# Kernel tuning notes

Hardware: AMD Instinct MI355X
Metric: run time of the kernel (lower is better)

Reference implementation:

```python
import jax, jax.numpy as jnp
import numpy as np

IS, OS, H = 168, 24, 256           # input window, output horizon, state_hsize
TAU, MAXIMUM = 0.1, 1.0            # tau parameter (non-grad) and series maximum
DILS = [[1, 4], [16, 64]]          # ResidualDRNN groups of dilations


def _lstm(x, wih, whh, bih, bhh):
    """Single-layer LSTM over time-major x: (T, B, C). PyTorch gate order i,f,g,o."""
    def step(carry, xt):
        h, c = carry
        g = xt @ wih.T + h @ whh.T + (bih + bhh)
        i, f, gg, o = jnp.split(g, 4, axis=-1)
        c = jax.nn.sigmoid(f) * c + jax.nn.sigmoid(i) * jnp.tanh(gg)
        h = jax.nn.sigmoid(o) * jnp.tanh(c)
        return (h, c), h
    h0 = jnp.zeros((x.shape[1], H), x.dtype)
    _, hs = jax.lax.scan(step, (h0, h0), x)
    return hs


def _dilated_lstm(x, d, p):
    """Standard DRNN layer: pad T to multiple of d, interleave time into batch, run LSTM."""
    T, B, C = x.shape
    n = -(-T // d)
    xp = jnp.pad(x, ((0, n * d - T), (0, 0), (0, 0)))
    hd = _lstm(xp.reshape(n, d * B, C), *p)
    return hd.reshape(n * d, B, H)[:T]


def _forward(train, init_lev_sm, lstm_params, nl_w, nl_b, sc_w, sc_b):
    B, T = train.shape
    a = jax.nn.sigmoid(init_lev_sm[0])            # lev_sms (idxs are all 0 -> same scalar)
    floor = TAU * MAXIMUM                          # tau * maximum
    # --- exponential-smoothing level recurrence (sequential) ---
    lev0 = jnp.maximum(train[:, 0], floor)
    def step(lev, xt):
        new = jnp.maximum(a * xt + (1.0 - a) * lev, floor)
        return new, new
    _, rest = jax.lax.scan(step, lev0, train[:, 1:].T)
    levs = jnp.concatenate([lev0[None], rest], axis=0).T   # [B, T]
    # --- windowed normalization ---
    w_idx = jnp.arange(IS - 1, T)                           # W = T - IS + 1 window ends
    in_win = train[:, (w_idx - IS + 1)[:, None] + jnp.arange(IS)[None, :]]
    in_win = (in_win / levs[:, w_idx][:, :, None]).transpose(1, 0, 2)    # [W, B, IS]
    o_idx = jnp.arange(IS - 1, T - OS)                      # W_out = T - OS - IS + 1
    out_win = train[:, (o_idx + 1)[:, None] + jnp.arange(OS)[None, :]]
    out_win = (out_win / levs[:, o_idx][:, :, None]).transpose(1, 0, 2)  # [W_out, B, OS]
    # --- ResidualDRNN stack on window_input[:-OS] (time-major: windows are the sequence) ---
    x = in_win[:-OS]
    li = 0
    for g, dils in enumerate(DILS):
        residual = x
        h = x
        for d in dils:
            h = _dilated_lstm(h, d, lstm_params[li])
            li += 1
        x = h + residual if g > 0 else h                    # dropout p=0 -> identity
    x = jnp.tanh(x @ nl_w.T + nl_b)                         # add_nl_layer
    pred = x @ sc_w.T + sc_b                                # scoring
    return pred, out_win


def setup_inputs() -> dict:
    key = jax.random.key(0)
    ks = list(jax.random.split(key, 32))
    B, T = 32, 1024
    inp = {
        "train": jax.random.uniform(ks[0], (B, T), jnp.float32, 0.05, 1.0),
        "val": jax.random.uniform(ks[1], (B, T), jnp.float32, 0.05, 1.0),
        "test": jax.random.uniform(ks[2], (B, T), jnp.float32, 0.05, 1.0),
        "idxs": jnp.zeros((B,), jnp.int32),
        "init_lev_sm": jnp.array([0.5], jnp.float32),
    }
    sizes = [IS, H, H, H]  # input feature size of each of the 4 DRNN layers
    k = 3
    s = 1.0 / np.sqrt(H)
    for i, cin in enumerate(sizes):
        inp[f"wih{i}"] = jax.random.uniform(ks[k], (4 * H, cin), jnp.float32, -s, s); k += 1
        inp[f"whh{i}"] = jax.random.uniform(ks[k], (4 * H, H), jnp.float32, -s, s); k += 1
        inp[f"bih{i}"] = jax.random.uniform(ks[k], (4 * H,), jnp.float32, -s, s); k += 1
        inp[f"bhh{i}"] = jax.random.uniform(ks[k], (4 * H,), jnp.float32, -s, s); k += 1
    inp["nl_w"] = jax.random.uniform(ks[k], (H, H), jnp.float32, -s, s); k += 1
    inp["nl_b"] = jnp.zeros((H,), jnp.float32)
    inp["sc_w"] = jax.random.uniform(ks[k], (OS, H), jnp.float32, -s, s); k += 1
    inp["sc_b"] = jnp.zeros((OS,), jnp.float32)
    return inp


def reference(train, val, test, idxs, init_lev_sm,
              wih0, whh0, bih0, bhh0, wih1, whh1, bih1, bhh1,
              wih2, whh2, bih2, bhh2, wih3, whh3, bih3, bhh3,
              nl_w, nl_b, sc_w, sc_b):
    lstm_params = [(wih0, whh0, bih0, bhh0), (wih1, whh1, bih1, bhh1),
                   (wih2, whh2, bih2, bhh2), (wih3, whh3, bih3, bhh3)]
    # training path (validating=False, testing=False): only `train` is used
    return _forward(train, init_lev_sm, lstm_params, nl_w, nl_b, sc_w, sc_b)
```

## Files before the change

kernel.cpp:

```cpp
#include <hip/hip_runtime.h>
#include <hip/hip_fp16.h>
#include <math.h>

#define TT 833
#define GDIM 1024

typedef _Float16 f16x8 __attribute__((ext_vector_type(8)));
typedef float    f32x4 __attribute__((ext_vector_type(4)));

#if __has_builtin(__builtin_amdgcn_rcpf)
__device__ __forceinline__ float frcp(float x){ return __builtin_amdgcn_rcpf(x); }
#else
__device__ __forceinline__ float frcp(float x){ return 1.f/x; }
#endif

#if __has_builtin(__builtin_amdgcn_sdot4)
__device__ __forceinline__ int sdot4(unsigned a, unsigned b, int c){
  return __builtin_amdgcn_sdot4((int)a, (int)b, c, false);
}
#else
__device__ __forceinline__ int sdot4(unsigned a, unsigned b, int c){
  int ai = (int)a, bi = (int)b;
  c += ((ai<<24)>>24)*((bi<<24)>>24);
  c += ((ai<<16)>>24)*((bi<<16)>>24);
  c += ((ai<<8)>>24)*((bi<<8)>>24);
  c += (ai>>24)*(bi>>24);
  return c;
}
#endif

__device__ __forceinline__ void lds_barrier(){
  asm volatile("s_waitcnt lgkmcnt(0)" ::: "memory");
  __builtin_amdgcn_s_barrier();
  __builtin_amdgcn_sched_barrier(0);
}


__global__ void levels_k(const float* __restrict__ train, const float* __restrict__ ism,
                         float* __restrict__ levs){
  int b = threadIdx.x;
  if (b >= 32) return;
  float a = 1.f/(1.f+expf(-ism[0]));
  const float4* tr4 = reinterpret_cast<const float4*>(train + b*1024);
  float4* lv4 = reinterpret_cast<float4*>(levs + b*1024);
  float lev = 0.f;
  for (int i = 0; i < 256; ++i){
    float4 v = tr4[i];
    float4 o;
    if (i == 0) o.x = lev = fmaxf(v.x, 0.1f);
    else        o.x = lev = fmaxf(fmaf(a, v.x, (1.f-a)*lev), 0.1f);
    o.y = lev = fmaxf(fmaf(a, v.y, (1.f-a)*lev), 0.1f);
    o.z = lev = fmaxf(fmaf(a, v.z, (1.f-a)*lev), 0.1f);
    o.w = lev = fmaxf(fmaf(a, v.w, (1.f-a)*lev), 0.1f);
    lv4[i] = o;
  }
}

__global__ void win_x_k(const float* __restrict__ train, const float* __restrict__ levs,
                        __half* __restrict__ x0){
  int idx = blockIdx.x*256 + threadIdx.x;
  int i = idx % 192;
  int r = idx / 192;
  int b = r & 31;
  int t = r >> 5;
  x0[idx] = (i < 168) ? __float2half(train[b*1024 + t + i] / levs[b*1024 + t + 167])
                      : __float2half(0.f);
}

__global__ void win_out_k(const float* __restrict__ train, const float* __restrict__ levs,
                          float* __restrict__ ow){
  int idx = blockIdx.x*256 + threadIdx.x;
  int o = idx % 24;
  int r = idx / 24;
  int b = r & 31;
  int t = r >> 5;
  ow[idx] = train[b*1024 + 168 + t + o] / levs[b*1024 + t + 167];
}

__global__ void permw_k(const float* __restrict__ wih, const float* __restrict__ bih,
                        const float* __restrict__ bhh, __half* __restrict__ wP,
                        float* __restrict__ bP, int K, int Kpad){
  int t = blockIdx.x;
  int g = ((t & 3) << 8) + (t >> 2);
  for (int k = threadIdx.x; k < Kpad; k += 256)
    wP[(size_t)t*Kpad + k] = (k < K) ? __float2half(wih[(size_t)g*K + k]) : __float2half(0.f);
  if (threadIdx.x == 0) bP[t] = bih[g] + bhh[g];
}

__global__ void cvth_k(const float* __restrict__ s, __half* __restrict__ d, int n){
  int i = blockIdx.x*256 + threadIdx.x;
  if (i < n) d[i] = __float2half(s[i]);
}

__global__ void packq_k(const float* __restrict__ w, uint4* __restrict__ wq,
                        float* __restrict__ sc){
  int t = blockIdx.x*256 + threadIdx.x;
  if (t >= 1024) return;
  int g = ((t & 3) << 8) + (t >> 2);
  const float* row = w + (size_t)g*256;
  float amax = 0.f;
  for (int k = 0; k < 256; ++k) amax = fmaxf(amax, fabsf(row[k]));
  amax = fmaxf(amax, 1e-20f);
  float s = amax/127.f, inv = 127.f/amax;
  sc[t] = s;
  for (int k16 = 0; k16 < 16; ++k16){
    union { uint4 u; signed char b[16]; } r;
    #pragma unroll
    for (int j = 0; j < 16; ++j){
      float q = rintf(row[k16*16 + j]*inv);
      q = fminf(fmaxf(q, -127.f), 127.f);
      r.b[j] = (signed char)q;
    }
    wq[(size_t)k16*1024 + t] = r.u;
  }
}

__global__ __launch_bounds__(512) void proj_mfma(
    const _Float16* __restrict__ A, const _Float16* __restrict__ W,
    const float* __restrict__ b1,
    void* __restrict__ C, int Mout, int K, int N, int dil, int act, int outHalf)
{
  __shared__ _Float16 As[256*40];
  __shared__ _Float16 Bs[128*40];
  const int tid = threadIdx.x;
  const int lane = tid & 63;
  const int w = tid >> 6, wr = w >> 1, wc = w & 1;
  const int m0 = blockIdx.y << 8, n0 = blockIdx.x << 7;

  const int rowA = tid >> 1;
  const int halfsel = tid & 1;
  int srcrow;
  {
    int m = m0 + rowA;
    if (dil == 0) srcrow = (m < Mout) ? m : -1;
    else {
      int rows = dil << 5;
      int jj = m / rows;
      int q = m - jj*rows;
      int t = jj*dil + (q >> 5);
      srcrow = (t < TT) ? ((t << 5) + (q & 31)) : -1;
    }
  }
  const int rowB = (tid & 255) >> 1;
  const int nrow = n0 + rowB;

  f32x4 acc[4][4];
  #pragma unroll
  for (int i = 0; i < 4; ++i)
    #pragma unroll
    for (int j = 0; j < 4; ++j) acc[i][j] = (f32x4){0.f,0.f,0.f,0.f};

  const int nkt = K >> 5;
  for (int kt = 0; kt < nkt; ++kt){
    const int k0 = (kt << 5) + halfsel*16;
    {
      union { uint4 u[2]; _Float16 h[16]; } tmp;
      if (srcrow >= 0){
        const uint4* s = reinterpret_cast<const uint4*>(A + (size_t)srcrow*K + k0);
        tmp.u[0] = s[0]; tmp.u[1] = s[1];
      } else {
        tmp.u[0] = make_uint4(0,0,0,0); tmp.u[1] = make_uint4(0,0,0,0);
      }
      uint4* dst = reinterpret_cast<uint4*>(&As[rowA*40 + halfsel*16]);
      dst[0] = tmp.u[0]; dst[1] = tmp.u[1];
    }
    if (tid < 256){
      const uint4* s = reinterpret_cast<const uint4*>(W + (size_t)nrow*K + k0);
      uint4* dst = reinterpret_cast<uint4*>(&Bs[rowB*40 + halfsel*16]);
      dst[0] = s[0]; dst[1] = s[1];
    }
    __syncthreads();
    {
      const int kg = lane >> 4, r16 = lane & 15;
      f16x8 af[4], bf[4];
      #pragma unroll
      for (int mi = 0; mi < 4; ++mi)
        af[mi] = *reinterpret_cast<const f16x8*>(&As[(wr*64 + mi*16 + r16)*40 + kg*8]);
      #pragma unroll
      for (int nj = 0; nj < 4; ++nj)
        bf[nj] = *reinterpret_cast<const f16x8*>(&Bs[(wc*64 + nj*16 + r16)*40 + kg*8]);
      #pragma unroll
      for (int mi = 0; mi < 4; ++mi)
        #pragma unroll
        for (int nj = 0; nj < 4; ++nj)
          acc[mi][nj] = __builtin_amdgcn_mfma_f32_16x16x32_f16(af[mi], bf[nj], acc[mi][nj], 0, 0, 0);
    }
    __syncthreads();
  }
  #pragma unroll
  for (int mi = 0; mi < 4; ++mi){
    #pragma unroll
    for (int p = 0; p < 4; ++p){
      int mrow = m0 + wr*64 + mi*16 + (lane >> 4)*4 + p;
      if (mrow >= Mout) continue;
      #pragma unroll
      for (int nj = 0; nj < 4; ++nj){
        int ncol = n0 + wc*64 + nj*16 + (lane & 15);
        float v = acc[mi][nj][p] + b1[ncol];
        if (act) v = tanhf(v);
        if (outHalf) reinterpret_cast<__half*>(C)[(size_t)mrow*N + ncol] = __float2half(v);
        else reinterpret_cast<float*>(C)[(size_t)mrow*N + ncol] = v;
      }
    }
  }
}

template<int NR>
__global__ __launch_bounds__(512, 1) void srecr2_k(
    const uint4* __restrict__ wq, const float* __restrict__ scale,
    const __half* __restrict__ Gin,
    __half* __restrict__ outh, float* __restrict__ outf,
    int nsteps, int d, int rowsTotal)
{
  __shared__ __align__(16) unsigned int hq[2][NR][64];
  const int tid = threadIdx.x;
  const int s = tid & 1;
  const int j = tid >> 1;
  const int q0 = blockIdx.x*NR;
  const float sg0 = scale[2*tid]*(1.f/127.f);
  const float sg1 = scale[2*tid + 1]*(1.f/127.f);
  uint4 w0_[16], w1_[16];
  #pragma unroll
  for (int kk = 0; kk < 16; ++kk){
    w0_[kk] = wq[(size_t)kk*1024 + 2*tid];
    w1_[kk] = wq[(size_t)kk*1024 + 2*tid + 1];
  }
  float c[NR];
  #pragma unroll
  for (int rr = 0; rr < NR; ++rr) c[rr] = 0.f;
  for (int e = tid; e < 2*NR*64; e += 512) (&hq[0][0][0])[e] = 0u;
  __syncthreads();

  for (int step = 0; step < nsteps; ++step){
    const int cur = step & 1;
    const __half2* gbase = reinterpret_cast<const __half2*>(
        Gin + ((size_t)step*rowsTotal + q0)*GDIM);
    #pragma unroll
    for (int rr = 0; rr < NR; ++rr){
      __half2 g2 = gbase[rr*512 + tid];
      float gin0 = __half2float(__low2half(g2));
      float gin1 = __half2float(__high2half(g2));
      int a00 = 0, a01 = 0, a10 = 0, a11 = 0;
      #pragma unroll
      for (int k16 = 0; k16 < 8; ++k16){
        uint4 ha = *reinterpret_cast<const uint4*>(&hq[cur][rr][4*k16]);
        a00 = sdot4(w0_[k16].x, ha.x, a00); a00 = sdot4(w0_[k16].y, ha.y, a00);
        a00 = sdot4(w0_[k16].z, ha.z, a00); a00 = sdot4(w0_[k16].w, ha.w, a00);
        a10 = sdot4(w1_[k16].x, ha.x, a10); a10 = sdot4(w1_[k16].y, ha.y, a10);
        a10 = sdot4(w1_[k16].z, ha.z, a10); a10 = sdot4(w1_[k16].w, ha.w, a10);
        uint4 hb = *reinterpret_cast<const uint4*>(&hq[cur][rr][4*(k16 + 8)]);
        a01 = sdot4(w0_[k16+8].x, hb.x, a01); a01 = sdot4(w0_[k16+8].y, hb.y, a01);
        a01 = sdot4(w0_[k16+8].z, hb.z, a01); a01 = sdot4(w0_[k16+8].w, hb.w, a01);
        a11 = sdot4(w1_[k16+8].x, hb.x, a11); a11 = sdot4(w1_[k16+8].y, hb.y, a11);
        a11 = sdot4(w1_[k16+8].w, hb.w, a11); a11 = sdot4(w1_[k16+8].z, hb.z, a11);
      }
      float p0 = fmaf((float)(a00 + a01), sg0, gin0);
      float p1 = fmaf((float)(a10 + a11), sg1, gin1);
      float px0 = s ? p0 + p0 : p0;
      float t0 = frcp(1.f + __expf(-px0));
      float a0v = s ? fmaf(2.f, t0, -1.f) : t0;
      float a1v = frcp(1.f + __expf(-p1));
      float b0 = __shfl_xor(a0v, 1);
      float b1 = __shfl_xor(a1v, 1);
      float iv = s ? b0 : a0v;
      float fv = s ? b1 : a1v;
      float gv = s ? a0v : b0;
      float ov = s ? a1v : b1;
      float cn = fmaf(fv, c[rr], iv*gv);
      c[rr] = cn;
      if (s == 0){
        float e2 = __expf(-2.f*cn);
        float h = ov*(1.f - e2)*frcp(1.f + e2);
        int qh = (int)rintf(h*127.f);
        reinterpret_cast<signed char*>(&hq[cur^1][rr][0])[j] = (signed char)qh;
        int q = q0 + rr;
        int tg = step*d + (q >> 5);
        if (tg < TT){
          size_t oi = ((size_t)tg*32 + (q & 31))*256 + j;
          outh[oi] = __float2half(h);
          if (outf) outf[oi] = h;
        }
      }
    }
    lds_barrier();
  }
}

template<int NR>
__global__ __launch_bounds__(1024) void srecq_k(
    const uint4* __restrict__ wq, const float* __restrict__ scale,
    const __half* __restrict__ Gin,
    __half* __restrict__ outh, const float* __restrict__ res,
    int nsteps, int d, int rowsTotal)
{
  __shared__ __align__(16) unsigned int hq[2][NR][64];
  const int tid = threadIdx.x;
  const int lane = tid & 63;
  const int base = lane & ~3;
  const int kg = tid & 3;
  const int j = tid >> 2;
  const int q0 = blockIdx.x*NR;
  const float sg = scale[tid]*(1.f/127.f);
  float c[NR];
  #pragma unroll
  for (int rr = 0; rr < NR; ++rr) c[rr] = 0.f;
  for (int e = tid; e < 2*NR*64; e += 1024) (&hq[0][0][0])[e] = 0u;
  __syncthreads();

  for (int step = 0; step < nsteps; ++step){
    const int cur = step & 1;
    float gin[NR];
    const __half* gbase = Gin + ((size_t)step*rowsTotal + q0)*GDIM;
    #pragma unroll
    for (int rr = 0; rr < NR; ++rr) gin[rr] = __half2float(gbase[rr*GDIM + tid]);
    int acc[NR];
    #pragma unroll
    for (int rr = 0; rr < NR; ++rr) acc[rr] = 0;
    #pragma unroll 4
    for (int k16 = 0; k16 < 16; ++k16){
      uint4 w = wq[(size_t)k16*1024 + tid];
      #pragma unroll
      for (int rr = 0; rr < NR; ++rr){
        uint4 h4 = *reinterpret_cast<const uint4*>(&hq[cur][rr][4*k16]);
        acc[rr] = sdot4(w.x, h4.x, acc[rr]);
        acc[rr] = sdot4(w.y, h4.y, acc[rr]);
        acc[rr] = sdot4(w.z, h4.z, acc[rr]);
        acc[rr] = sdot4(w.w, h4.w, acc[rr]);
      }
    }
    #pragma unroll
    for (int rr = 0; rr < NR; ++rr){
      float p = fmaf((float)acc[rr], sg, gin[rr]);
      float px = (kg == 2) ? p + p : p;
      float sv = frcp(1.f + __expf(-px));
      float a = (kg == 2) ? fmaf(2.f, sv, -1.f) : sv;
      float iv = __shfl(a, base + 0);
      float fv = __shfl(a, base + 1);
      float gv = __shfl(a, base + 2);
      float ov = __shfl(a, base + 3);
      float cn = fmaf(fv, c[rr], iv*gv);
      c[rr] = cn;
      float e2 = __expf(-2.f*cn);
      float h = ov*(1.f - e2)*frcp(1.f + e2);
      if (kg == 0){
        int qh = (int)rintf(h*127.f);
        reinterpret_cast<signed char*>(&hq[cur^1][rr][0])[j] = (signed char)qh;
        int q = q0 + rr;
        int tg = step*d + (q >> 5);
        if (tg < TT){
          size_t oi = ((size_t)tg*32 + (q & 31))*256 + j;
          outh[oi] = __float2half(h + res[oi]);
        }
      }
    }
    lds_barrier();
  }
}

__global__ __launch_bounds__(256) void sc_head(const __half* __restrict__ xt, const float* __restrict__ w,
                        const float* __restrict__ bias, float* __restrict__ outp, int M){
  __shared__ float arow[8][256];
  int m0 = blockIdx.x << 3;
  int tid = threadIdx.x;
  #pragma unroll
  for (int i = 0; i < 8; ++i){
    int e = tid + (i << 8);
    int r = e >> 8, k = e & 255;
    arow[r][k] = (m0 + r < M) ? __half2float(xt[(size_t)(m0 + r)*256 + k]) : 0.f;
  }
  __syncthreads();
  int r = tid >> 5, n = tid & 31;
  if (n < 24 && (m0 + r) < M){
    float acc = bias[n];
    const float* wr = w + n*256;
    #pragma unroll 8
    for (int k = 0; k < 256; ++k) acc = fmaf(arow[r][k], wr[k], acc);
    outp[(size_t)(m0 + r)*24 + n] = acc;
  }
}

extern "C" void kernel_launch(void* const* d_in, const int* in_sizes, int n_in,
                              void* d_out, int out_size, void* d_ws, size_t ws_size,
                              hipStream_t stream){
  const float* train = (const float*)d_in[0];
  const float* ism   = (const float*)d_in[4];
  const float* wih[4] = {(const float*)d_in[5], (const float*)d_in[9], (const float*)d_in[13], (const float*)d_in[17]};
  const float* whh[4] = {(const float*)d_in[6], (const float*)d_in[10], (const float*)d_in[14], (const float*)d_in[18]};
  const float* bih[4] = {(const float*)d_in[7], (const float*)d_in[11], (const float*)d_in[15], (const float*)d_in[19]};
  const float* bhh[4] = {(const float*)d_in[8], (const float*)d_in[12], (const float*)d_in[16], (const float*)d_in[20]};
  const float* nl_w = (const float*)d_in[21];
  const float* nl_b = (const float*)d_in[22];
  const float* sc_w = (const float*)d_in[23];
  const float* sc_b = (const float*)d_in[24];
  float* out = (float*)d_out;

  float* ws = (float*)d_ws;
  size_t off = 0;
  float* levs = ws + off;   off += 32768;
  uint4* wqk[4];
  for (int l = 0; l < 4; ++l){ wqk[l] = (uint4*)(ws + off); off += 65536; }
  float* sck[4];
  for (int l = 0; l < 4; ++l){ sck[l] = ws + off; off += 1024; }
  __half* wPh[4];
  for (int l = 0; l < 4; ++l){ wPh[l] = (__half*)(ws + off); off += 131072; }
  float* bP[4];
  for (int l = 0; l < 4; ++l){ bP[l] = ws + off; off += 1024; }
  __half* nlwh = (__half*)(ws + off); off += 32768;
  __half* x0h = (__half*)(ws + off);  off += (size_t)26656*192/2;
  __half* G   = (__half*)(ws + off);  off += (size_t)28672*1024/2;
  __half* h0h = (__half*)(ws + off);  off += (size_t)26656*256/2;
  __half* h1h = (__half*)(ws + off);  off += (size_t)26656*256/2;
  float*  h1f = ws + off;             off += (size_t)26656*256;
  __half* h2h = (__half*)(ws + off);  off += (size_t)26656*256/2;
  __half* xfh = (__half*)(ws + off);  off += (size_t)26656*256/2;
  __half* xth = (__half*)(ws + off);  off += (size_t)26656*256/2;
  (void)ws_size; (void)in_sizes; (void)n_in; (void)out_size;

  levels_k<<<1, 64, 0, stream>>>(train, ism, levs);
  win_x_k<<<19992, 256, 0, stream>>>(train, levs, x0h);
  win_out_k<<<2499, 256, 0, stream>>>(train, levs, out + 639744);
  const int Kin[4]  = {168, 256, 256, 256};
  const int Kpad[4] = {192, 256, 256, 256};
  for (int l = 0; l < 4; ++l){
    packq_k<<<4, 256, 0, stream>>>(whh[l], wqk[l], sck[l]);
    permw_k<<<1024, 256, 0, stream>>>(wih[l], bih[l], bhh[l], wPh[l], bP[l], Kin[l], Kpad[l]);
  }
  cvth_k<<<256, 256, 0, stream>>>(nl_w, nlwh, 65536);

  proj_mfma<<<dim3(8,105), 512, 0, stream>>>((const _Float16*)x0h, (const _Float16*)wPh[0], bP[0], G, 26656, 192, 1024, 0, 0, 1);
  srecr2_k<1><<<32, 512, 0, stream>>>(wqk[0], sck[0], G, h0h, nullptr, 833, 1, 32);
  proj_mfma<<<dim3(8,105), 512, 0, stream>>>((const _Float16*)h0h, (const _Float16*)wPh[1], bP[1], G, 26752, 256, 1024, 4, 0, 1);
  srecr2_k<1><<<128, 512, 0, stream>>>(wqk[1], sck[1], G, h1h, h1f, 209, 4, 128);
  proj_mfma<<<dim3(8,106), 512, 0, stream>>>((const _Float16*)h1h, (const _Float16*)wPh[2], bP[2], G, 27136, 256, 1024, 16, 0, 1);
  srecr2_k<2><<<256, 512, 0, stream>>>(wqk[2], sck[2], G, h2h, nullptr, 53, 16, 512);
  proj_mfma<<<dim3(8,112), 512, 0, stream>>>((const _Float16*)h2h, (const _Float16*)wPh[3], bP[3], G, 28672, 256, 1024, 64, 0, 1);
  srecq_k<8><<<256, 1024, 0, stream>>>(wqk[3], sck[3], G, xfh, h1f, 14, 64, 2048);
  proj_mfma<<<dim3(2,105), 512, 0, stream>>>((const _Float16*)xfh, (const _Float16*)nlwh, nl_b, xth, 26656, 256, 256, 0, 1, 1);
  sc_head<<<3332, 256, 0, stream>>>(xth, sc_w, sc_b, out, 26656);
}
```

Before: 1.613 ms.

## Compute all four LSTM gates per thread in recurrent kernel, halving block size

The recurrent int8-dot kernel now gives each of 256 threads one hidden unit with all four gates (i,f,g,o) held in registers, instead of 512 threads each handling two gates and exchanging them by cross-lane shuffles. This removes the shuffles and the idle half of threads in the cell-update tail, and every thread now writes h. The cost is twice as many weight registers per thread (64 uint4) and a longer serial dot-product chain per thread, with fewer waves available to hide latency on the sequential critical path.

```diff
diff --git a/kernel.cpp b/kernel.cpp
--- a/kernel.cpp
+++ b/kernel.cpp
@@ -206,80 +206,75 @@
 }
 
 template<int NR>
-__global__ __launch_bounds__(512, 1) void srecr2_k(
+__global__ __launch_bounds__(256, 1) void srecc_k(
     const uint4* __restrict__ wq, const float* __restrict__ scale,
     const __half* __restrict__ Gin,
     __half* __restrict__ outh, float* __restrict__ outf,
     int nsteps, int d, int rowsTotal)
 {
   __shared__ __align__(16) unsigned int hq[2][NR][64];
-  const int tid = threadIdx.x;
-  const int s = tid & 1;
-  const int j = tid >> 1;
+  const int t = threadIdx.x;
   const int q0 = blockIdx.x*NR;
-  const float sg0 = scale[2*tid]*(1.f/127.f);
-  const float sg1 = scale[2*tid + 1]*(1.f/127.f);
-  uint4 w0_[16], w1_[16];
-  #pragma unroll
-  for (int kk = 0; kk < 16; ++kk){
-    w0_[kk] = wq[(size_t)kk*1024 + 2*tid];
-    w1_[kk] = wq[(size_t)kk*1024 + 2*tid + 1];
-  }
+  float sg[4];
+  #pragma unroll
+  for (int g = 0; g < 4; ++g) sg[g] = scale[4*t + g]*(1.f/127.f);
+  uint4 w_[4][16];
+  #pragma unroll
+  for (int k = 0; k < 16; ++k)
+    #pragma unroll
+    for (int g = 0; g < 4; ++g)
+      w_[g][k] = wq[(size_t)k*1024 + 4*t + g];
   float c[NR];
   #pragma unroll
   for (int rr = 0; rr < NR; ++rr) c[rr] = 0.f;
-  for (int e = tid; e < 2*NR*64; e += 512) (&hq[0][0][0])[e] = 0u;
+  for (int e = t; e < 2*NR*64; e += 256) (&hq[0][0][0])[e] = 0u;
   __syncthreads();
 
   for (int step = 0; step < nsteps; ++step){
     const int cur = step & 1;
-    const __half2* gbase = reinterpret_cast<const __half2*>(
-        Gin + ((size_t)step*rowsTotal + q0)*GDIM);
     #pragma unroll
     for (int rr = 0; rr < NR; ++rr){
-      __half2 g2 = gbase[rr*512 + tid];
-      float gin0 = __half2float(__low2half(g2));
-      float gin1 = __half2float(__high2half(g2));
-      int a00 = 0, a01 = 0, a10 = 0, a11 = 0;
-      #pragma unroll
-      for (int k16 = 0; k16 < 8; ++k16){
-        uint4 ha = *reinterpret_cast<const uint4*>(&hq[cur][rr][4*k16]);
-        a00 = sdot4(w0_[k16].x, ha.x, a00); a00 = sdot4(w0_[k16].y, ha.y, a00);
-        a00 = sdot4(w0_[k16].z, ha.z, a00); a00 = sdot4(w0_[k16].w, ha.w, a00);
-        a10 = sdot4(w1_[k16].x, ha.x, a10); a10 = sdot4(w1_[k16].y, ha.y, a10);
-        a10 = sdot4(w1_[k16].z, ha.z, a10); a10 = sdot4(w1_[k16].w, ha.w, a10);
-        uint4 hb = *reinterpret_cast<const uint4*>(&hq[cur][rr][4*(k16 + 8)]);
-        a01 = sdot4(w0_[k16+8].x, hb.x, a01); a01 = sdot4(w0_[k16+8].y, hb.y, a01);
-        a01 = sdot4(w0_[k16+8].z, hb.z, a01); a01 = sdot4(w0_[k16+8].w, hb.w, a01);
-        a11 = sdot4(w1_[k16+8].x, hb.x, a11); a11 = sdot4(w1_[k16+8].y, hb.y, a11);
-        a11 = sdot4(w1_[k16+8].w, hb.w, a11); a11 = sdot4(w1_[k16+8].z, hb.z, a11);
-      }
-      float p0 = fmaf((float)(a00 + a01), sg0, gin0);
-      float p1 = fmaf((float)(a10 + a11), sg1, gin1);
-      float px0 = s ? p0 + p0 : p0;
-      float t0 = frcp(1.f + __expf(-px0));
-      float a0v = s ? fmaf(2.f, t0, -1.f) : t0;
-      float a1v = frcp(1.f + __expf(-p1));
-      float b0 = __shfl_xor(a0v, 1);
-      float b1 = __shfl_xor(a1v, 1);
-      float iv = s ? b0 : a0v;
-      float fv = s ? b1 : a1v;
-      float gv = s ? a0v : b0;
-      float ov = s ? a1v : b1;
+      const __half* gb = Gin + ((size_t)step*rowsTotal + q0 + rr)*GDIM + 4*t;
+      uint2 gu = *reinterpret_cast<const uint2*>(gb);
+      union { unsigned u; __half2 h2; } glo, ghi;
+      glo.u = gu.x; ghi.u = gu.y;
+      float gi = __half2float(__low2half(glo.h2));
+      float gf = __half2float(__high2half(glo.h2));
+      float gg = __half2float(__low2half(ghi.h2));
+      float go = __half2float(__high2half(ghi.h2));
+      int a0 = 0, a1 = 0, a2 = 0, a3 = 0;
+      #pragma unroll
+      for (int k = 0; k < 16; ++k){
+        uint4 h4 = *reinterpret_cast<const uint4*>(&hq[cur][rr][4*k]);
+        a0 = sdot4(w_[0][k].x, h4.x, a0); a0 = sdot4(w_[0][k].y, h4.y, a0);
+        a0 = sdot4(w_[0][k].z, h4.z, a0); a0 = sdot4(w_[0][k].w, h4.w, a0);
+        a1 = sdot4(w_[1][k].x, h4.x, a1); a1 = sdot4(w_[1][k].y, h4.y, a1);
+        a1 = sdot4(w_[1][k].z, h4.z, a1); a1 = sdot4(w_[1][k].w, h4.w, a1);
+        a2 = sdot4(w_[2][k].x, h4.x, a2); a2 = sdot4(w_[2][k].y, h4.y, a2);
+        a2 = sdot4(w_[2][k].z, h4.z, a2); a2 = sdot4(w_[2][k].w, h4.w, a2);
+        a3 = sdot4(w_[3][k].x, h4.x, a3); a3 = sdot4(w_[3][k].y, h4.y, a3);
+        a3 = sdot4(w_[3][k].z, h4.z, a3); a3 = sdot4(w_[3][k].w, h4.w, a3);
+      }
+      float pi = fmaf((float)a0, sg[0], gi);
+      float pf = fmaf((float)a1, sg[1], gf);
+      float pg = fmaf((float)a2, sg[2], gg);
+      float po = fmaf((float)a3, sg[3], go);
+      float iv = frcp(1.f + __expf(-pi));
+      float fv = frcp(1.f + __expf(-pf));
+      float gv = fmaf(2.f, frcp(1.f + __expf(-2.f*pg)), -1.f);
+      float ov = frcp(1.f + __expf(-po));
       float cn = fmaf(fv, c[rr], iv*gv);
       c[rr] = cn;
-      if (s == 0){
-        float e2 = __expf(-2.f*cn);
-        float h = ov*(1.f - e2)*frcp(1.f + e2);
-        int qh = (int)rintf(h*127.f);
-        reinterpret_cast<signed char*>(&hq[cur^1][rr][0])[j] = (signed char)qh;
-        int q = q0 + rr;
-        int tg = step*d + (q >> 5);
-        if (tg < TT){
-          size_t oi = ((size_t)tg*32 + (q & 31))*256 + j;
-          outh[oi] = __float2half(h);
-          if (outf) outf[oi] = h;
-        }
+      float e2 = __expf(-2.f*cn);
+      float h = ov*(1.f - e2)*frcp(1.f + e2);
+      int qh = (int)rintf(h*127.f);
+      reinterpret_cast<signed char*>(&hq[cur^1][rr][0])[t] = (signed char)qh;
+      int q = q0 + rr;
+      int tg = step*d + (q >> 5);
+      if (tg < TT){
+        size_t oi = ((size_t)tg*32 + (q & 31))*256 + t;
+        outh[oi] = __float2half(h);
+        if (outf) outf[oi] = h;
       }
     }
     lds_barrier();
@@ -428,11 +423,11 @@
   cvth_k<<<256, 256, 0, stream>>>(nl_w, nlwh, 65536);
 
   proj_mfma<<<dim3(8,105), 512, 0, stream>>>((const _Float16*)x0h, (const _Float16*)wPh[0], bP[0], G, 26656, 192, 1024, 0, 0, 1);
-  srecr2_k<1><<<32, 512, 0, stream>>>(wqk[0], sck[0], G, h0h, nullptr, 833, 1, 32);
+  srecc_k<1><<<32, 256, 0, stream>>>(wqk[0], sck[0], G, h0h, nullptr, 833, 1, 32);
   proj_mfma<<<dim3(8,105), 512, 0, stream>>>((const _Float16*)h0h, (const _Float16*)wPh[1], bP[1], G, 26752, 256, 1024, 4, 0, 1);
-  srecr2_k<1><<<128, 512, 0, stream>>>(wqk[1], sck[1], G, h1h, h1f, 209, 4, 128);
+  srecc_k<1><<<128, 256, 0, stream>>>(wqk[1], sck[1], G, h1h, h1f, 209, 4, 128);
   proj_mfma<<<dim3(8,106), 512, 0, stream>>>((const _Float16*)h1h, (const _Float16*)wPh[2], bP[2], G, 27136, 256, 1024, 16, 0, 1);
-  srecr2_k<2><<<256, 512, 0, stream>>>(wqk[2], sck[2], G, h2h, nullptr, 53, 16, 512);
+  srecc_k<2><<<256, 256, 0, stream>>>(wqk[2], sck[2], G, h2h, nullptr, 53, 16, 512);
   proj_mfma<<<dim3(8,112), 512, 0, stream>>>((const _Float16*)h2h, (const _Float16*)wPh[3], bP[3], G, 28672, 256, 1024, 64, 0, 1);
   srecq_k<8><<<256, 1024, 0, stream>>>(wqk[3], sck[3], G, xfh, h1f, 14, 64, 2048);
   proj_mfma<<<dim3(2,105), 512, 0, stream>>>((const _Float16*)xfh, (const _Float16*)nlwh, nl_b, xth, 26656, 256, 256, 0, 1, 1);
```

New measurement: 2.368 ms. 1.47x slower.
